# Optimization experiments

Hardware: AMD Instinct MI355X
Metric: run time of the kernel (lower is better)

Reference implementation:

```python
import jax, jax.numpy as jnp
import numpy as np

B, T, N, K, C = 4, 12, 2000, 8, 32
AGG_N = 4  # mean, max, min, std
EPS = 1e-5


def sparsify(a, k):
    # keep top-k entries per row, zero the rest (torch.topk + torch.where)
    thr = jax.lax.top_k(a, k)[0][..., -1:]
    return jnp.where(a < thr, jnp.zeros_like(a), a)


def aggregate(I, adj):
    # I: (b,t,n,f), adj: (b,n,n) row-sparsified with K nonzeros per row
    deg = jnp.sum(adj, axis=-1)[:, None, :, None]              # (b,1,n,1)
    mean = jnp.einsum('bnm,btmf->btnf', adj, I) / deg
    meansq = jnp.einsum('bnm,btmf->btnf', adj, I * I) / deg
    std = jnp.sqrt(jax.nn.relu(meansq - mean * mean) + EPS)
    vals, idx = jax.lax.top_k(adj, K)                          # (b,n,K)
    nb = jax.vmap(lambda Ib, ib: Ib[:, ib])(I, idx)            # (b,t,n,K,f)
    valid = (vals > 0)[:, None, :, :, None]
    mx = jnp.max(jnp.where(valid, nb, -jnp.inf), axis=3)
    mn = jnp.min(jnp.where(valid, nb, jnp.inf), axis=3)
    return jnp.concatenate([mean, mx, mn, std], axis=3)


def stower(x, adj, Theta, bias, masking, use_scalers):
    # x: (b,c,t,n) -> out: (b,o,t,n)
    I = jnp.transpose(x, (0, 2, 3, 1))                          # (b,t,n,c)
    m = aggregate(I, adj)
    if masking:
        m = jnp.where(jnp.isnan(m), 6.0, m)
        m = jnp.where(jnp.isinf(m), 0.0, m)
        m = jnp.minimum(m, 6.0)
    if use_scalers:
        deg = jnp.sum((adj > 0).astype(m.dtype), axis=-1)       # (b,n)
        s = jnp.log1p(deg)[:, None, :, None]
        m = jnp.concatenate([m, m * s, m / s], axis=3)
    out = jnp.einsum('btji,io->btjo', m, Theta) + bias
    return jnp.transpose(out, (0, 3, 1, 2))


def tcn(x, W, b):
    # tcn_layer2 with act='linear': tanh(conv1x1(x) + x)
    return jnp.tanh(jnp.einsum('oc,bctn->botn', W, x) + b[None, :, None, None] + x)


def setup_inputs():
    key = jax.random.key(0)
    ks = jax.random.split(key, 14)
    stdv = 1.0 / np.sqrt(C)
    u = lambda k, shape: jax.random.uniform(k, shape, jnp.float32, -stdv, stdv)
    return {
        'X': jax.random.normal(ks[0], (B, T, N, 1), jnp.float32),
        'adj': jax.random.uniform(ks[1], (N, N), jnp.float32),
        'adj_mask': jax.random.uniform(ks[2], (N, N), jnp.float32),
        'Theta0': u(ks[3], (AGG_N * 1, C)),   # len(agg)*len(['identity'])*in_variables
        'bias0': u(ks[4], (C,)),
        'Wt0': u(ks[5], (C, C)),
        'bt0': u(ks[6], (C,)),
        'Theta1': u(ks[7], (AGG_N * 3 * C, C)),  # len(agg)*len(scalers)*channels
        'bias1': u(ks[8], (C,)),
        'Wt1': u(ks[9], (C, C)),
        'bt1': u(ks[10], (C,)),
        'Wout': u(ks[11], (1, C)),
        'bout': u(ks[12], (1,)),
        'batch_seen': 0,
        'epoch': 0,
        'train': 0,
    }


def reference(X, adj, adj_mask, Theta0, bias0, Wt0, bt0, Theta1, bias1, Wt1, bt1, Wout, bout, batch_seen, epoch, train):
    x0 = X[:, None, :, :, 0]                                   # (b,1,t,n)
    adj_s = sparsify(jnp.broadcast_to(adj, (B, N, N)), K)
    adjm_s = sparsify(jnp.broadcast_to(adj_mask, (B, N, N)), K)
    h = stower(x0, adjm_s, Theta0, bias0, True, False)         # s_layer0 (masking, identity scaler)
    h = tcn(h, Wt0, bt0)                                       # t_layer0
    h = jax.nn.relu(stower(h, adj_s, Theta1, bias1, False, True))
    h = jax.nn.relu(tcn(h, Wt1, bt1))
    y = jnp.einsum('oc,bctn->botn', Wout, h) + bout[None, :, None, None]
    return y.reshape(B, T, N)
```

## Files before the change

### kernel.cpp

```cpp
#include <hip/hip_runtime.h>
#include <hip/hip_bf16.h>
#include <math.h>

#define BB 4
#define TT 12
#define NN 2000
#define KK 8
#define CC 32
#define EPSF 1e-5f
#define LISTCAP 16
#define NSITES (BB * TT * NN)
#define MACRO 32
#define NMACRO (NSITES / MACRO)
#define GRID_C 1000

typedef unsigned short u16;
typedef __bf16 bf16x8 __attribute__((ext_vector_type(8)));
typedef float  f32x4  __attribute__((ext_vector_type(4)));

union bfpack { bf16x8 v; u16 u[8]; };

__device__ __forceinline__ u16 f2bf(float x) {
    union { __hip_bfloat16 h; u16 u; } c;
    c.h = __float2bfloat16(x);
    return c.u;
}
__device__ __forceinline__ float bf2f(u16 u) {
    return __uint_as_float(((unsigned)u) << 16);
}
__device__ __forceinline__ float mask6(float v) {
    if (isnan(v)) v = 6.0f;
    if (isinf(v)) v = 0.0f;
    return fminf(v, 6.0f);
}
__device__ __forceinline__ unsigned long long shflx64(unsigned long long v, int m) {
    int lo = __shfl_xor((int)(unsigned)(v & 0xffffffffull), m, 64);
    int hi = __shfl_xor((int)(unsigned)(v >> 32), m, 64);
    return ((unsigned long long)(unsigned)hi << 32) | (unsigned)lo;
}

__global__ __launch_bounds__(256)
void topk_prep(const float* __restrict__ adj, const float* __restrict__ adjm,
               int* __restrict__ t_idx, float* __restrict__ t_val,
               int* __restrict__ t_cnt, float* __restrict__ t_deg,
               float* __restrict__ t_ideg, float2* __restrict__ t_sc)
{
    __shared__ int wext[4][8];
    __shared__ int wextn[4];
    const int tid = threadIdx.x;
    const int wid = tid >> 6, lane = tid & 63;
    if (lane == 0) wextn[wid] = 0;

    const int grow = blockIdx.x * 4 + wid;
    const int mat = (grow >= NN) ? 1 : 0;
    const int row = grow - mat * NN;
    const float* src = (mat == 0 ? adjm : adj) + (size_t)row * NN;

    unsigned long long key[8];
    #pragma unroll
    for (int j = 0; j < 8; ++j) key[j] = 0ull;

    for (int i = lane; i < NN; i += 64) {
        float v = src[i];
        unsigned long long nk =
            ((unsigned long long)__float_as_uint(v) << 32) | (unsigned)(~(unsigned)i);
        if (nk > key[7]) {
            #pragma unroll
            for (int j = 7; j >= 1; --j)
                key[j] = (nk > key[j - 1]) ? key[j - 1] : ((nk > key[j]) ? nk : key[j]);
            if (nk > key[0]) key[0] = nk;
        }
    }

    #pragma unroll
    for (int d = 1; d < 64; d <<= 1) {
        unsigned long long ok[8], c[8];
        #pragma unroll
        for (int j = 0; j < 8; ++j) ok[j] = shflx64(key[j], d);
        #pragma unroll
        for (int j = 0; j < 8; ++j) {
            unsigned long long o = ok[7 - j];
            c[j] = (key[j] > o) ? key[j] : o;
        }
        #pragma unroll
        for (int st = 4; st >= 1; st >>= 1) {
            #pragma unroll
            for (int j = 0; j < 8; ++j) {
                if ((j & st) == 0 && (j | st) < 8) {
                    unsigned long long a = c[j], b = c[j | st];
                    unsigned long long hi = (a > b) ? a : b;
                    unsigned long long lo = (a > b) ? b : a;
                    c[j] = hi; c[j | st] = lo;
                }
            }
        }
        #pragma unroll
        for (int j = 0; j < 8; ++j) key[j] = c[j];
    }

    const float thr = __uint_as_float((unsigned)(key[7] >> 32));

    float degp = 0.f; int cp = 0;
    for (int i = lane; i < NN; i += 64) {
        float v = src[i];
        if (v >= thr) {
            degp += v;
            if (v > 0.f) cp++;
            if (v == thr) {
                unsigned long long nk =
                    ((unsigned long long)__float_as_uint(v) << 32) | (unsigned)(~(unsigned)i);
                if (nk < key[7]) {
                    int p = atomicAdd(&wextn[wid], 1);
                    if (p < 8) wext[wid][p] = i;
                }
            }
        }
    }
    #pragma unroll
    for (int off = 32; off >= 1; off >>= 1) {
        degp += __shfl_xor(degp, off, 64);
        cp   += __shfl_xor(cp, off, 64);
    }
    __syncthreads();

    if (lane == 0) {
        int en = wextn[wid]; if (en > 8) en = 8;
        const size_t ob = (size_t)grow * LISTCAP;
        #pragma unroll
        for (int j = 0; j < 8; ++j) {
            t_idx[ob + j] = (int)(~(unsigned)(key[j] & 0xffffffffull));
            t_val[ob + j] = __uint_as_float((unsigned)(key[j] >> 32));
        }
        for (int j = 0; j < 8; ++j) {
            t_idx[ob + 8 + j] = (j < en) ? wext[wid][j] : 0;
            t_val[ob + 8 + j] = (j < en) ? thr : 0.f;
        }
        t_cnt[grow]  = 8 + en;
        t_deg[grow]  = degp;
        t_ideg[grow] = 1.0f / degp;
        float s1 = log1pf((float)cp);
        t_sc[grow]   = make_float2(s1, 1.0f / s1);
    }
}

__global__ __launch_bounds__(256)
void stower0_tcn0(const float* __restrict__ X,
                  const int* __restrict__ t_idx, const float* __restrict__ t_val,
                  const int* __restrict__ t_cnt, const float* __restrict__ t_deg,
                  const float* __restrict__ Theta0, const float* __restrict__ bias0,
                  const float* __restrict__ Wt0, const float* __restrict__ bt0,
                  float* __restrict__ I1)
{
    const int site = blockIdx.x * 256 + threadIdx.x;
    const int n  = site % NN;
    const int bt = site / NN;
    const float* xrow = X + (size_t)bt * NN;

    const size_t base = (size_t)n * LISTCAP;
    const int cnt   = t_cnt[n];
    const float deg = t_deg[n];
    float wsum = 0.f, wsq = 0.f, mx = -INFINITY, mn = INFINITY;
    for (int j = 0; j < cnt; ++j) {
        int   id = t_idx[base + j];
        float w  = t_val[base + j];
        float xv = xrow[id];
        wsum = fmaf(w, xv, wsum);
        wsq  = fmaf(w * xv, xv, wsq);
        if (j < KK && w > 0.f) { mx = fmaxf(mx, xv); mn = fminf(mn, xv); }
    }
    float mean = wsum / deg;
    float var  = wsq / deg - mean * mean;
    float sd   = sqrtf(fmaxf(var, 0.f) + EPSF);
    float m0 = mask6(mean), m1 = mask6(mx), m2 = mask6(mn), m3 = mask6(sd);

    float h0[CC];
    #pragma unroll
    for (int c = 0; c < CC; ++c) {
        float v = bias0[c];
        v = fmaf(m0, Theta0[0 * CC + c], v);
        v = fmaf(m1, Theta0[1 * CC + c], v);
        v = fmaf(m2, Theta0[2 * CC + c], v);
        v = fmaf(m3, Theta0[3 * CC + c], v);
        h0[c] = v;
    }
    float* op = I1 + (size_t)site * CC;
    #pragma unroll
    for (int c = 0; c < CC; ++c) {
        float acc = bt0[c] + h0[c];
        #pragma unroll
        for (int k = 0; k < CC; ++k) acc = fmaf(Wt0[c * CC + k], h0[k], acc);
        op[c] = tanhf(acc);
    }
}

__global__ __launch_bounds__(256, 3)
void stower1_tcn1_out(const float* __restrict__ I1,
                      const int* __restrict__ t_idx, const float* __restrict__ t_val,
                      const int* __restrict__ t_cnt, const float* __restrict__ t_ideg,
                      const float2* __restrict__ t_sc,
                      const float* __restrict__ Theta1, const float* __restrict__ bias1,
                      const float* __restrict__ Wt1, const float* __restrict__ bt1,
                      const float* __restrict__ Wout, const float* __restrict__ bout,
                      float* __restrict__ out)
{
    __shared__ u16 sBlo[96 * 128];
    __shared__ alignas(16) char uSpace[24576];
    __shared__ float sPart[64];

    u16*   stage = (u16*)uSpace;
    u16*   sAhi  = (u16*)uSpace;
    u16*   sAlo  = sAhi + 32 * 128;
    u16*   hHi   = (u16*)uSpace;
    u16*   hLo   = hHi + 32 * 40;
    float* h32   = (float*)(uSpace + 5120);

    const int tid  = threadIdx.x;
    const int lane = tid & 63;
    const int w    = tid >> 6;
    const int m15  = lane & 15;
    const int q    = lane >> 4;
    const int sl   = tid >> 5;
    const int f    = tid & 31;
    const int hf   = w & 1;
    const int st   = w >> 1;
    const int ot   = w >> 1;
    const int st2  = w & 1;

    for (int i = tid; i < 384 * 32; i += 256) {
        const int row = i >> 5, o = i & 31;
        const int jm = row >> 7, k = row & 127;
        const int nt = jm * 2 + (o >> 4), n = o & 15;
        stage[(nt * 16 + n) * 128 + (((k >> 3) ^ n) << 3) + (k & 7)] = f2bf(Theta1[i]);
    }
    __syncthreads();
    bf16x8 bH[3][4];
    #pragma unroll
    for (int j3 = 0; j3 < 3; ++j3) {
        const int tile = 2 * j3 + hf;
        #pragma unroll
        for (int ks = 0; ks < 4; ++ks)
            bH[j3][ks] = *(const bf16x8*)&stage[(tile * 16 + m15) * 128 +
                                                (((ks * 4 + q) ^ m15) << 3)];
    }
    __syncthreads();
    for (int i = tid; i < 384 * 32; i += 256) {
        const int row = i >> 5, o = i & 31;
        const int jm = row >> 7, k = row & 127;
        const int nt = jm * 2 + (o >> 4), n = o & 15;
        const float v = Theta1[i];
        const u16 hi = f2bf(v);
        sBlo[(nt * 16 + n) * 128 + (((k >> 3) ^ n) << 3) + (k & 7)] = f2bf(v - bf2f(hi));
    }
    bfpack bwh, bwl;
    {
        const float* wp = &Wt1[(ot * 16 + m15) * CC + q * 8];
        const float4 v0 = *(const float4*)wp;
        const float4 v1 = *(const float4*)(wp + 4);
        const float vv[8] = {v0.x, v0.y, v0.z, v0.w, v1.x, v1.y, v1.z, v1.w};
        #pragma unroll
        for (int j = 0; j < 8; ++j) {
            const u16 hi = f2bf(vv[j]);
            bwh.u[j] = hi;
            bwl.u[j] = f2bf(vv[j] - bf2f(hi));
        }
    }
    const float b1o   = bias1[hf * 16 + m15];
    const float bt1o  = bt1[ot * 16 + m15];
    const float wouto = Wout[ot * 16 + m15];
    const float boutv = bout[0];

    for (int mb = blockIdx.x; mb < NMACRO; mb += GRID_C) {
        const int sbase = mb * MACRO;

        #pragma unroll
        for (int it = 0; it < 4; ++it) {
            const int s = it * 8 + sl;
            const int site = sbase + s;
            const int n  = site % NN;
            const int bt = site / NN;
            const size_t rbase = (size_t)(NN + n) * LISTCAP;
            const int cnt    = t_cnt[NN + n];
            const float ideg = t_ideg[NN + n];
            const float* Ibt = I1 + (size_t)bt * NN * CC;

            const int4   i0 = *(const int4*)&t_idx[rbase];
            const int4   i1 = *(const int4*)&t_idx[rbase + 4];
            const float4 w0 = *(const float4*)&t_val[rbase];
            const float4 w1 = *(const float4*)&t_val[rbase + 4];

            const float x0 = Ibt[(size_t)i0.x * CC + f];
            const float x1 = Ibt[(size_t)i0.y * CC + f];
            const float x2 = Ibt[(size_t)i0.z * CC + f];
            const float x3 = Ibt[(size_t)i0.w * CC + f];
            const float x4 = Ibt[(size_t)i1.x * CC + f];
            const float x5 = Ibt[(size_t)i1.y * CC + f];
            const float x6 = Ibt[(size_t)i1.z * CC + f];
            const float x7 = Ibt[(size_t)i1.w * CC + f];

            float wsum = 0.f, wsq = 0.f, mx = -INFINITY, mn = INFINITY;
            #define AGG(wv, xv) do { \
                wsum = fmaf(wv, xv, wsum); wsq = fmaf(wv * xv, xv, wsq); \
                mx = fmaxf(mx, xv); mn = fminf(mn, xv); } while (0)
            AGG(w0.x, x0); AGG(w0.y, x1); AGG(w0.z, x2); AGG(w0.w, x3);
            AGG(w1.x, x4); AGG(w1.y, x5); AGG(w1.z, x6); AGG(w1.w, x7);
            #undef AGG
            if (cnt > 8) {
                for (int j = 8; j < cnt; ++j) {
                    int   id = t_idx[rbase + j];
                    float wv = t_val[rbase + j];
                    float xv = Ibt[(size_t)id * CC + f];
                    wsum = fmaf(wv, xv, wsum);
                    wsq  = fmaf(wv * xv, xv, wsq);
                }
            }
            const float mean = wsum * ideg;
            const float var  = wsq * ideg - mean * mean;
            const float sd   = sqrtf(fmaxf(var, 0.f) + EPSF);

            const int sx = s & 15;
            const int b  = s * 128;
            const int fh = f >> 3, fl = f & 7;
            const int ia  = b + (((0  + fh) ^ sx) << 3) + fl;
            const int ib  = b + (((4  + fh) ^ sx) << 3) + fl;
            const int ic  = b + (((8  + fh) ^ sx) << 3) + fl;
            const int id_ = b + (((12 + fh) ^ sx) << 3) + fl;
            u16 h0 = f2bf(mean); sAhi[ia]  = h0; sAlo[ia]  = f2bf(mean - bf2f(h0));
            u16 h1 = f2bf(mx);   sAhi[ib]  = h1; sAlo[ib]  = f2bf(mx   - bf2f(h1));
            u16 h2 = f2bf(mn);   sAhi[ic]  = h2; sAlo[ic]  = f2bf(mn   - bf2f(h2));
            u16 h3 = f2bf(sd);   sAhi[id_] = h3; sAlo[id_] = f2bf(sd   - bf2f(h3));
        }
        __syncthreads();

        f32x4 acc[3];
        #pragma unroll
        for (int j3 = 0; j3 < 3; ++j3) acc[j3] = (f32x4){0.f, 0.f, 0.f, 0.f};

        const int arow = (st * 16 + m15) * 128;
        #pragma unroll
        for (int ks = 0; ks < 4; ++ks) {
            const int koff = (((ks * 4 + q) ^ m15) << 3);
            const bf16x8 aH = *(const bf16x8*)&sAhi[arow + koff];
            const bf16x8 aL = *(const bf16x8*)&sAlo[arow + koff];
            #pragma unroll
            for (int j3 = 0; j3 < 3; ++j3) {
                const bf16x8 bL = *(const bf16x8*)&sBlo[((2 * j3 + hf) * 16 + m15) * 128 + koff];
                acc[j3] = __builtin_amdgcn_mfma_f32_16x16x32_bf16(aH, bH[j3][ks], acc[j3], 0, 0, 0);
                acc[j3] = __builtin_amdgcn_mfma_f32_16x16x32_bf16(aH, bL,          acc[j3], 0, 0, 0);
                acc[j3] = __builtin_amdgcn_mfma_f32_16x16x32_bf16(aL, bH[j3][ks], acc[j3], 0, 0, 0);
            }
        }
        __syncthreads();

        #pragma unroll
        for (int r = 0; r < 4; ++r) {
            const int sl2  = st * 16 + q * 4 + r;
            const int site = sbase + sl2;
            const int n    = site % NN;
            const float2 sc = t_sc[NN + n];
            float h = acc[0][r] + sc.x * acc[1][r] + sc.y * acc[2][r] + b1o;
            h = fmaxf(h, 0.f);
            const int o = hf * 16 + m15;
            const u16 hi = f2bf(h);
            hHi[sl2 * 40 + o] = hi;
            hLo[sl2 * 40 + o] = f2bf(h - bf2f(hi));
            h32[sl2 * 33 + o] = h;
        }
        __syncthreads();

        f32x4 c2 = (f32x4){0.f, 0.f, 0.f, 0.f};
        {
            const bf16x8 ahh = *(const bf16x8*)&hHi[(st2 * 16 + m15) * 40 + q * 8];
            const bf16x8 ahl = *(const bf16x8*)&hLo[(st2 * 16 + m15) * 40 + q * 8];
            c2 = __builtin_amdgcn_mfma_f32_16x16x32_bf16(ahh, bwh.v, c2, 0, 0, 0);
            c2 = __builtin_amdgcn_mfma_f32_16x16x32_bf16(ahh, bwl.v, c2, 0, 0, 0);
            c2 = __builtin_amdgcn_mfma_f32_16x16x32_bf16(ahl, bwh.v, c2, 0, 0, 0);
        }
        float p[4];
        #pragma unroll
        for (int r = 0; r < 4; ++r) {
            const int sl2 = st2 * 16 + q * 4 + r;
            const float hres = h32[sl2 * 33 + ot * 16 + m15];
            float yv = tanhf(c2[r] + bt1o + hres);
            yv = fmaxf(yv, 0.f);
            p[r] = yv * wouto;
            #pragma unroll
            for (int mk = 1; mk <= 8; mk <<= 1)
                p[r] += __shfl_xor(p[r], mk, 64);
        }
        float selv  = (m15 & 1) ? p[1] : p[0];
        float selv2 = (m15 & 1) ? p[3] : p[2];
        selv = (m15 & 2) ? selv2 : selv;
        if (m15 < 4) sPart[ot * 32 + st2 * 16 + q * 4 + m15] = selv;
        __syncthreads();

        if (tid < 32) out[sbase + tid] = sPart[tid] + sPart[32 + tid] + boutv;
    }
}

extern "C" void kernel_launch(void* const* d_in, const int* in_sizes, int n_in,
                              void* d_out, int out_size, void* d_ws, size_t ws_size,
                              hipStream_t stream)
{
    const float* X      = (const float*)d_in[0];
    const float* adj    = (const float*)d_in[1];
    const float* adjm   = (const float*)d_in[2];
    const float* Theta0 = (const float*)d_in[3];
    const float* bias0  = (const float*)d_in[4];
    const float* Wt0    = (const float*)d_in[5];
    const float* bt0    = (const float*)d_in[6];
    const float* Theta1 = (const float*)d_in[7];
    const float* bias1  = (const float*)d_in[8];
    const float* Wt1    = (const float*)d_in[9];
    const float* bt1    = (const float*)d_in[10];
    const float* Wout   = (const float*)d_in[11];
    const float* bout   = (const float*)d_in[12];
    (void)in_sizes; (void)n_in; (void)out_size; (void)ws_size;

    char* p = (char*)d_ws;
    int*    t_idx  = (int*)p;    p += (size_t)2 * NN * LISTCAP * sizeof(int);
    float*  t_val  = (float*)p;  p += (size_t)2 * NN * LISTCAP * sizeof(float);
    int*    t_cnt  = (int*)p;    p += (size_t)2 * NN * sizeof(int);
    float*  t_deg  = (float*)p;  p += (size_t)2 * NN * sizeof(float);
    float*  t_ideg = (float*)p;  p += (size_t)2 * NN * sizeof(float);
    float2* t_sc   = (float2*)p; p += (size_t)2 * NN * sizeof(float2);
    float*  I1     = (float*)p;  p += (size_t)NSITES * CC * sizeof(float);

    hipLaunchKernelGGL(topk_prep, dim3(2 * NN / 4), dim3(256), 0, stream,
                       adj, adjm, t_idx, t_val, t_cnt, t_deg, t_ideg, t_sc);
    hipLaunchKernelGGL(stower0_tcn0, dim3(NSITES / 256), dim3(256), 0, stream,
                       X, t_idx, t_val, t_cnt, t_deg, Theta0, bias0, Wt0, bt0, I1);
    hipLaunchKernelGGL(stower1_tcn1_out, dim3(GRID_C), dim3(256), 0, stream,
                       I1, t_idx, t_val, t_cnt, t_ideg, t_sc,
                       Theta1, bias1, Wt1, bt1, Wout, bout, (float*)d_out);
}
```

Measured before the change: 200.0 us.

## Split fused layer-1 kernel into separate aggregation and GEMM kernels

Splits the persistent fused stower1/tcn1/output kernel into two launches. An aggregation kernel gathers neighbours and writes the swizzled hi/lo bf16 features to a global workspace. A GEMM kernel then reads them back and runs the MFMA projection, tcn and output reduction, one 32-site tile per block. The aim is to drop the persistent loop and shrink the LDS footprint for more parallelism and occupancy. In exchange it adds a large global round-trip for the intermediate features and makes every block rebuild the Theta1 tiles in LDS.

```diff
diff --git a/kernel.cpp b/kernel.cpp
--- a/kernel.cpp
+++ b/kernel.cpp
@@ -10,9 +10,6 @@
 #define EPSF 1e-5f
 #define LISTCAP 16
 #define NSITES (BB * TT * NN)
-#define MACRO 32
-#define NMACRO (NSITES / MACRO)
-#define GRID_C 1000
 
 typedef unsigned short u16;
 typedef __bf16 bf16x8 __attribute__((ext_vector_type(8)));
@@ -193,34 +190,88 @@
     }
 }
 
-__global__ __launch_bounds__(256, 3)
-void stower1_tcn1_out(const float* __restrict__ I1,
-                      const int* __restrict__ t_idx, const float* __restrict__ t_val,
-                      const int* __restrict__ t_cnt, const float* __restrict__ t_ideg,
-                      const float2* __restrict__ t_sc,
-                      const float* __restrict__ Theta1, const float* __restrict__ bias1,
-                      const float* __restrict__ Wt1, const float* __restrict__ bt1,
-                      const float* __restrict__ Wout, const float* __restrict__ bout,
-                      float* __restrict__ out)
+__global__ __launch_bounds__(256)
+void stower1_agg(const float* __restrict__ I1,
+                 const int* __restrict__ t_idx, const float* __restrict__ t_val,
+                 const int* __restrict__ t_cnt, const float* __restrict__ t_ideg,
+                 u16* __restrict__ mHi, u16* __restrict__ mLo)
 {
-    __shared__ u16 sBlo[96 * 128];
-    __shared__ alignas(16) char uSpace[24576];
+    const int tid  = threadIdx.x;
+    const int site = blockIdx.x * 8 + (tid >> 5);
+    const int f    = tid & 31;
+    const int n  = site % NN;
+    const int bt = site / NN;
+    const size_t rbase = (size_t)(NN + n) * LISTCAP;
+    const int cnt    = t_cnt[NN + n];
+    const float ideg = t_ideg[NN + n];
+    const float* Ibt = I1 + (size_t)bt * NN * CC;
+
+    const int4   i0 = *(const int4*)&t_idx[rbase];
+    const int4   i1 = *(const int4*)&t_idx[rbase + 4];
+    const float4 w0 = *(const float4*)&t_val[rbase];
+    const float4 w1 = *(const float4*)&t_val[rbase + 4];
+
+    const float x0 = Ibt[(size_t)i0.x * CC + f];
+    const float x1 = Ibt[(size_t)i0.y * CC + f];
+    const float x2 = Ibt[(size_t)i0.z * CC + f];
+    const float x3 = Ibt[(size_t)i0.w * CC + f];
+    const float x4 = Ibt[(size_t)i1.x * CC + f];
+    const float x5 = Ibt[(size_t)i1.y * CC + f];
+    const float x6 = Ibt[(size_t)i1.z * CC + f];
+    const float x7 = Ibt[(size_t)i1.w * CC + f];
+
+    float wsum = 0.f, wsq = 0.f, mx = -INFINITY, mn = INFINITY;
+    #define AGG(wv, xv) do { \
+        wsum = fmaf(wv, xv, wsum); wsq = fmaf(wv * xv, xv, wsq); \
+        mx = fmaxf(mx, xv); mn = fminf(mn, xv); } while (0)
+    AGG(w0.x, x0); AGG(w0.y, x1); AGG(w0.z, x2); AGG(w0.w, x3);
+    AGG(w1.x, x4); AGG(w1.y, x5); AGG(w1.z, x6); AGG(w1.w, x7);
+    #undef AGG
+    if (cnt > 8) {
+        for (int j = 8; j < cnt; ++j) {
+            int   id = t_idx[rbase + j];
+            float wv = t_val[rbase + j];
+            float xv = Ibt[(size_t)id * CC + f];
+            wsum = fmaf(wv, xv, wsum);
+            wsq  = fmaf(wv * xv, xv, wsq);
+        }
+    }
+    const float mean = wsum * ideg;
+    const float var  = wsq * ideg - mean * mean;
+    const float sd   = sqrtf(fmaxf(var, 0.f) + EPSF);
+
+    const int sx = site & 15;
+    const int b  = site * 128;
+    const int fh = f >> 3, fl = f & 7;
+    const int ia  = b + (((0  + fh) ^ sx) << 3) + fl;
+    const int ib  = b + (((4  + fh) ^ sx) << 3) + fl;
+    const int ic  = b + (((8  + fh) ^ sx) << 3) + fl;
+    const int id_ = b + (((12 + fh) ^ sx) << 3) + fl;
+    u16 h0 = f2bf(mean); mHi[ia]  = h0; mLo[ia]  = f2bf(mean - bf2f(h0));
+    u16 h1 = f2bf(mx);   mHi[ib]  = h1; mLo[ib]  = f2bf(mx   - bf2f(h1));
+    u16 h2 = f2bf(mn);   mHi[ic]  = h2; mLo[ic]  = f2bf(mn   - bf2f(h2));
+    u16 h3 = f2bf(sd);   mHi[id_] = h3; mLo[id_] = f2bf(sd   - bf2f(h3));
+}
+
+__global__ __launch_bounds__(256)
+void stower1_gemm(const u16* __restrict__ mHi, const u16* __restrict__ mLo,
+                  const float2* __restrict__ t_sc,
+                  const float* __restrict__ Theta1, const float* __restrict__ bias1,
+                  const float* __restrict__ Wt1, const float* __restrict__ bt1,
+                  const float* __restrict__ Wout, const float* __restrict__ bout,
+                  float* __restrict__ out)
+{
+    __shared__ u16 sB[96 * 128];
+    __shared__ u16 hHi[32 * 40];
+    __shared__ u16 hLo[32 * 40];
+    __shared__ float h32[32 * 33];
     __shared__ float sPart[64];
-
-    u16*   stage = (u16*)uSpace;
-    u16*   sAhi  = (u16*)uSpace;
-    u16*   sAlo  = sAhi + 32 * 128;
-    u16*   hHi   = (u16*)uSpace;
-    u16*   hLo   = hHi + 32 * 40;
-    float* h32   = (float*)(uSpace + 5120);
 
     const int tid  = threadIdx.x;
     const int lane = tid & 63;
     const int w    = tid >> 6;
     const int m15  = lane & 15;
     const int q    = lane >> 4;
-    const int sl   = tid >> 5;
-    const int f    = tid & 31;
     const int hf   = w & 1;
     const int st   = w >> 1;
     const int ot   = w >> 1;
@@ -230,7 +281,7 @@
         const int row = i >> 5, o = i & 31;
         const int jm = row >> 7, k = row & 127;
         const int nt = jm * 2 + (o >> 4), n = o & 15;
-        stage[(nt * 16 + n) * 128 + (((k >> 3) ^ n) << 3) + (k & 7)] = f2bf(Theta1[i]);
+        sB[(nt * 16 + n) * 128 + (((k >> 3) ^ n) << 3) + (k & 7)] = f2bf(Theta1[i]);
     }
     __syncthreads();
     bf16x8 bH[3][4];
@@ -239,8 +290,8 @@
         const int tile = 2 * j3 + hf;
         #pragma unroll
         for (int ks = 0; ks < 4; ++ks)
-            bH[j3][ks] = *(const bf16x8*)&stage[(tile * 16 + m15) * 128 +
-                                                (((ks * 4 + q) ^ m15) << 3)];
+            bH[j3][ks] = *(const bf16x8*)&sB[(tile * 16 + m15) * 128 +
+                                             (((ks * 4 + q) ^ m15) << 3)];
     }
     __syncthreads();
     for (int i = tid; i < 384 * 32; i += 256) {
@@ -249,7 +300,7 @@
         const int nt = jm * 2 + (o >> 4), n = o & 15;
         const float v = Theta1[i];
         const u16 hi = f2bf(v);
-        sBlo[(nt * 16 + n) * 128 + (((k >> 3) ^ n) << 3) + (k & 7)] = f2bf(v - bf2f(hi));
+        sB[(nt * 16 + n) * 128 + (((k >> 3) ^ n) << 3) + (k & 7)] = f2bf(v - bf2f(hi));
     }
     bfpack bwh, bwl;
     {
@@ -268,133 +319,72 @@
     const float bt1o  = bt1[ot * 16 + m15];
     const float wouto = Wout[ot * 16 + m15];
     const float boutv = bout[0];
-
-    for (int mb = blockIdx.x; mb < NMACRO; mb += GRID_C) {
-        const int sbase = mb * MACRO;
-
-        #pragma unroll
-        for (int it = 0; it < 4; ++it) {
-            const int s = it * 8 + sl;
-            const int site = sbase + s;
-            const int n  = site % NN;
-            const int bt = site / NN;
-            const size_t rbase = (size_t)(NN + n) * LISTCAP;
-            const int cnt    = t_cnt[NN + n];
-            const float ideg = t_ideg[NN + n];
-            const float* Ibt = I1 + (size_t)bt * NN * CC;
-
-            const int4   i0 = *(const int4*)&t_idx[rbase];
-            const int4   i1 = *(const int4*)&t_idx[rbase + 4];
-            const float4 w0 = *(const float4*)&t_val[rbase];
-            const float4 w1 = *(const float4*)&t_val[rbase + 4];
-
-            const float x0 = Ibt[(size_t)i0.x * CC + f];
-            const float x1 = Ibt[(size_t)i0.y * CC + f];
-            const float x2 = Ibt[(size_t)i0.z * CC + f];
-            const float x3 = Ibt[(size_t)i0.w * CC + f];
-            const float x4 = Ibt[(size_t)i1.x * CC + f];
-            const float x5 = Ibt[(size_t)i1.y * CC + f];
-            const float x6 = Ibt[(size_t)i1.z * CC + f];
-            const float x7 = Ibt[(size_t)i1.w * CC + f];
-
-            float wsum = 0.f, wsq = 0.f, mx = -INFINITY, mn = INFINITY;
-            #define AGG(wv, xv) do { \
-                wsum = fmaf(wv, xv, wsum); wsq = fmaf(wv * xv, xv, wsq); \
-                mx = fmaxf(mx, xv); mn = fminf(mn, xv); } while (0)
-            AGG(w0.x, x0); AGG(w0.y, x1); AGG(w0.z, x2); AGG(w0.w, x3);
-            AGG(w1.x, x4); AGG(w1.y, x5); AGG(w1.z, x6); AGG(w1.w, x7);
-            #undef AGG
-            if (cnt > 8) {
-                for (int j = 8; j < cnt; ++j) {
-                    int   id = t_idx[rbase + j];
-                    float wv = t_val[rbase + j];
-                    float xv = Ibt[(size_t)id * CC + f];
-                    wsum = fmaf(wv, xv, wsum);
-                    wsq  = fmaf(wv * xv, xv, wsq);
-                }
-            }
-            const float mean = wsum * ideg;
-            const float var  = wsq * ideg - mean * mean;
-            const float sd   = sqrtf(fmaxf(var, 0.f) + EPSF);
-
-            const int sx = s & 15;
-            const int b  = s * 128;
-            const int fh = f >> 3, fl = f & 7;
-            const int ia  = b + (((0  + fh) ^ sx) << 3) + fl;
-            const int ib  = b + (((4  + fh) ^ sx) << 3) + fl;
-            const int ic  = b + (((8  + fh) ^ sx) << 3) + fl;
-            const int id_ = b + (((12 + fh) ^ sx) << 3) + fl;
-            u16 h0 = f2bf(mean); sAhi[ia]  = h0; sAlo[ia]  = f2bf(mean - bf2f(h0));
-            u16 h1 = f2bf(mx);   sAhi[ib]  = h1; sAlo[ib]  = f2bf(mx   - bf2f(h1));
-            u16 h2 = f2bf(mn);   sAhi[ic]  = h2; sAlo[ic]  = f2bf(mn   - bf2f(h2));
-            u16 h3 = f2bf(sd);   sAhi[id_] = h3; sAlo[id_] = f2bf(sd   - bf2f(h3));
-        }
-        __syncthreads();
-
-        f32x4 acc[3];
-        #pragma unroll
-        for (int j3 = 0; j3 < 3; ++j3) acc[j3] = (f32x4){0.f, 0.f, 0.f, 0.f};
-
-        const int arow = (st * 16 + m15) * 128;
-        #pragma unroll
-        for (int ks = 0; ks < 4; ++ks) {
-            const int koff = (((ks * 4 + q) ^ m15) << 3);
-            const bf16x8 aH = *(const bf16x8*)&sAhi[arow + koff];
-            const bf16x8 aL = *(const bf16x8*)&sAlo[arow + koff];
-            #pragma unroll
-            for (int j3 = 0; j3 < 3; ++j3) {
-                const bf16x8 bL = *(const bf16x8*)&sBlo[((2 * j3 + hf) * 16 + m15) * 128 + koff];
-                acc[j3] = __builtin_amdgcn_mfma_f32_16x16x32_bf16(aH, bH[j3][ks], acc[j3], 0, 0, 0);
-                acc[j3] = __builtin_amdgcn_mfma_f32_16x16x32_bf16(aH, bL,          acc[j3], 0, 0, 0);
-                acc[j3] = __builtin_amdgcn_mfma_f32_16x16x32_bf16(aL, bH[j3][ks], acc[j3], 0, 0, 0);
-            }
-        }
-        __syncthreads();
-
-        #pragma unroll
-        for (int r = 0; r < 4; ++r) {
-            const int sl2  = st * 16 + q * 4 + r;
-            const int site = sbase + sl2;
-            const int n    = site % NN;
-            const float2 sc = t_sc[NN + n];
-            float h = acc[0][r] + sc.x * acc[1][r] + sc.y * acc[2][r] + b1o;
-            h = fmaxf(h, 0.f);
-            const int o = hf * 16 + m15;
-            const u16 hi = f2bf(h);
-            hHi[sl2 * 40 + o] = hi;
-            hLo[sl2 * 40 + o] = f2bf(h - bf2f(hi));
-            h32[sl2 * 33 + o] = h;
-        }
-        __syncthreads();
-
-        f32x4 c2 = (f32x4){0.f, 0.f, 0.f, 0.f};
-        {
-            const bf16x8 ahh = *(const bf16x8*)&hHi[(st2 * 16 + m15) * 40 + q * 8];
-            const bf16x8 ahl = *(const bf16x8*)&hLo[(st2 * 16 + m15) * 40 + q * 8];
-            c2 = __builtin_amdgcn_mfma_f32_16x16x32_bf16(ahh, bwh.v, c2, 0, 0, 0);
-            c2 = __builtin_amdgcn_mfma_f32_16x16x32_bf16(ahh, bwl.v, c2, 0, 0, 0);
-            c2 = __builtin_amdgcn_mfma_f32_16x16x32_bf16(ahl, bwh.v, c2, 0, 0, 0);
-        }
-        float p[4];
-        #pragma unroll
-        for (int r = 0; r < 4; ++r) {
-            const int sl2 = st2 * 16 + q * 4 + r;
-            const float hres = h32[sl2 * 33 + ot * 16 + m15];
-            float yv = tanhf(c2[r] + bt1o + hres);
-            yv = fmaxf(yv, 0.f);
-            p[r] = yv * wouto;
-            #pragma unroll
-            for (int mk = 1; mk <= 8; mk <<= 1)
-                p[r] += __shfl_xor(p[r], mk, 64);
-        }
-        float selv  = (m15 & 1) ? p[1] : p[0];
-        float selv2 = (m15 & 1) ? p[3] : p[2];
-        selv = (m15 & 2) ? selv2 : selv;
-        if (m15 < 4) sPart[ot * 32 + st2 * 16 + q * 4 + m15] = selv;
-        __syncthreads();
-
-        if (tid < 32) out[sbase + tid] = sPart[tid] + sPart[32 + tid] + boutv;
-    }
+    __syncthreads();
+
+    const int sbase = blockIdx.x * 32;
+
+    f32x4 acc[3];
+    #pragma unroll
+    for (int j3 = 0; j3 < 3; ++j3) acc[j3] = (f32x4){0.f, 0.f, 0.f, 0.f};
+
+    const int arow = (sbase + st * 16 + m15) * 128;
+    #pragma unroll
+    for (int ks = 0; ks < 4; ++ks) {
+        const int koff = (((ks * 4 + q) ^ m15) << 3);
+        const bf16x8 aH = *(const bf16x8*)&mHi[arow + koff];
+        const bf16x8 aL = *(const bf16x8*)&mLo[arow + koff];
+        #pragma unroll
+        for (int j3 = 0; j3 < 3; ++j3) {
+            const bf16x8 bL = *(const bf16x8*)&sB[((2 * j3 + hf) * 16 + m15) * 128 + koff];
+            acc[j3] = __builtin_amdgcn_mfma_f32_16x16x32_bf16(aH, bH[j3][ks], acc[j3], 0, 0, 0);
+            acc[j3] = __builtin_amdgcn_mfma_f32_16x16x32_bf16(aH, bL,          acc[j3], 0, 0, 0);
+            acc[j3] = __builtin_amdgcn_mfma_f32_16x16x32_bf16(aL, bH[j3][ks], acc[j3], 0, 0, 0);
+        }
+    }
+
+    #pragma unroll
+    for (int r = 0; r < 4; ++r) {
+        const int sl2  = st * 16 + q * 4 + r;
+        const int site = sbase + sl2;
+        const int n    = site % NN;
+        const float2 sc = t_sc[NN + n];
+        float h = acc[0][r] + sc.x * acc[1][r] + sc.y * acc[2][r] + b1o;
+        h = fmaxf(h, 0.f);
+        const int o = hf * 16 + m15;
+        const u16 hi = f2bf(h);
+        hHi[sl2 * 40 + o] = hi;
+        hLo[sl2 * 40 + o] = f2bf(h - bf2f(hi));
+        h32[sl2 * 33 + o] = h;
+    }
+    __syncthreads();
+
+    f32x4 c2 = (f32x4){0.f, 0.f, 0.f, 0.f};
+    {
+        const bf16x8 ahh = *(const bf16x8*)&hHi[(st2 * 16 + m15) * 40 + q * 8];
+        const bf16x8 ahl = *(const bf16x8*)&hLo[(st2 * 16 + m15) * 40 + q * 8];
+        c2 = __builtin_amdgcn_mfma_f32_16x16x32_bf16(ahh, bwh.v, c2, 0, 0, 0);
+        c2 = __builtin_amdgcn_mfma_f32_16x16x32_bf16(ahh, bwl.v, c2, 0, 0, 0);
+        c2 = __builtin_amdgcn_mfma_f32_16x16x32_bf16(ahl, bwh.v, c2, 0, 0, 0);
+    }
+    float p[4];
+    #pragma unroll
+    for (int r = 0; r < 4; ++r) {
+        const int sl2 = st2 * 16 + q * 4 + r;
+        const float hres = h32[sl2 * 33 + ot * 16 + m15];
+        float yv = tanhf(c2[r] + bt1o + hres);
+        yv = fmaxf(yv, 0.f);
+        p[r] = yv * wouto;
+        #pragma unroll
+        for (int mk = 1; mk <= 8; mk <<= 1)
+            p[r] += __shfl_xor(p[r], mk, 64);
+    }
+    float selv  = (m15 & 1) ? p[1] : p[0];
+    float selv2 = (m15 & 1) ? p[3] : p[2];
+    selv = (m15 & 2) ? selv2 : selv;
+    if (m15 < 4) sPart[ot * 32 + st2 * 16 + q * 4 + m15] = selv;
+    __syncthreads();
+
+    if (tid < 32) out[sbase + tid] = sPart[tid] + sPart[32 + tid] + boutv;
 }
 
 extern "C" void kernel_launch(void* const* d_in, const int* in_sizes, int n_in,
@@ -424,12 +414,16 @@
     float*  t_ideg = (float*)p;  p += (size_t)2 * NN * sizeof(float);
     float2* t_sc   = (float2*)p; p += (size_t)2 * NN * sizeof(float2);
     float*  I1     = (float*)p;  p += (size_t)NSITES * CC * sizeof(float);
+    u16*    mHi    = (u16*)p;    p += (size_t)NSITES * 128 * sizeof(u16);
+    u16*    mLo    = (u16*)p;    p += (size_t)NSITES * 128 * sizeof(u16);
 
     hipLaunchKernelGGL(topk_prep, dim3(2 * NN / 4), dim3(256), 0, stream,
                        adj, adjm, t_idx, t_val, t_cnt, t_deg, t_ideg, t_sc);
     hipLaunchKernelGGL(stower0_tcn0, dim3(NSITES / 256), dim3(256), 0, stream,
                        X, t_idx, t_val, t_cnt, t_deg, Theta0, bias0, Wt0, bt0, I1);
-    hipLaunchKernelGGL(stower1_tcn1_out, dim3(GRID_C), dim3(256), 0, stream,
-                       I1, t_idx, t_val, t_cnt, t_ideg, t_sc,
-                       Theta1, bias1, Wt1, bt1, Wout, bout, (float*)d_out);
-}
+    hipLaunchKernelGGL(stower1_agg, dim3(NSITES / 8), dim3(256), 0, stream,
+                       I1, t_idx, t_val, t_cnt, t_ideg, mHi, mLo);
+    hipLaunchKernelGGL(stower1_gemm, dim3(NSITES / 32), dim3(256), 0, stream,
+                       mHi, mLo, t_sc, Theta1, bias1, Wt1, bt1, Wout, bout,
+                       (float*)d_out);
+}
```

Result: slower. 218.6 us (+9.3%).
